# Kernel tuning notes

Hardware: AMD Instinct MI355X
Metric: run time of the kernel (lower is better)

Reference implementation:

```python
import jax, jax.numpy as jnp
import numpy as np

SEQ = 4096
EMB = 1024
OUT = 1024


def setup_inputs() -> dict:
    key = jax.random.key(0)
    k_x, k_q, k_k, k_v = jax.random.split(key, 4)
    scale = 1.0 / np.sqrt(EMB)
    inputs = jax.random.normal(k_x, (SEQ, EMB), dtype=jnp.float32)
    # torch Linear weight is (out_features, in_features); y = x @ W.T
    W_Q = jax.random.normal(k_q, (OUT, EMB), dtype=jnp.float32) * scale
    W_K = jax.random.normal(k_k, (OUT, EMB), dtype=jnp.float32) * scale
    W_V = jax.random.normal(k_v, (OUT, EMB), dtype=jnp.float32) * scale
    return {"inputs": inputs, "W_Q": W_Q, "W_K": W_K, "W_V": W_V}


def reference(inputs, W_Q, W_K, W_V):
    # projections: (S, E) @ (E, D) -> (S, D)
    q = inputs @ W_Q.T
    k = inputs @ W_K.T
    v = inputs @ W_V.T
    d_k = k.shape[-1]
    scores = (q @ k.T) / jnp.sqrt(jnp.asarray(d_k, dtype=q.dtype))  # (S, S)
    weights = jax.nn.softmax(scores, axis=-1)
    return weights @ v  # (S, D)
```

## Files before the change

kernel.cpp:

```cpp
#include <hip/hip_runtime.h>

typedef __bf16 bf16;
typedef __bf16 bf16x4 __attribute__((ext_vector_type(4)));
typedef __bf16 bf16x8 __attribute__((ext_vector_type(8)));
typedef float f32x4 __attribute__((ext_vector_type(4)));

#define SEQ 4096
#define EMB 1024

#define MODE_BF16 0
#define MODE_EXP  1
#define MODE_PART 2

__device__ __forceinline__ void async_copy16(void* lds, const void* g) {
    __builtin_amdgcn_global_load_lds(
        (const __attribute__((address_space(1))) unsigned int*)g,
        (__attribute__((address_space(3))) unsigned int*)lds,
        16, 0, 0);
}

__global__ __launch_bounds__(256) void prep_all(const float* __restrict__ x,
                                                const float* __restrict__ wq,
                                                const float* __restrict__ wk,
                                                const float* __restrict__ wv,
                                                bf16* __restrict__ xb,
                                                bf16* __restrict__ wqk,
                                                bf16* __restrict__ wvb,
                                                float* __restrict__ rowsum)
{
    const int u = blockIdx.x * 256 + threadIdx.x;
    const float* src;
    bf16* dst;
    int off;
    if (u < 1048576)      { src = x;  dst = xb;               off = u; }
    else if (u < 1310720) { src = wq; dst = wqk;              off = u - 1048576; }
    else if (u < 1572864) { src = wk; dst = wqk + EMB * EMB;  off = u - 1310720; }
    else if (u < 1835008) { src = wv; dst = wvb;              off = u - 1572864; }
    else {
        *(float4*)(rowsum + (size_t)(u - 1835008) * 4) = float4{0.f, 0.f, 0.f, 0.f};
        return;
    }
    float4 f = *(const float4*)(src + (size_t)off * 4);
    bf16x4 v = { (bf16)f.x, (bf16)f.y, (bf16)f.z, (bf16)f.w };
    *(bf16x4*)(dst + (size_t)off * 4) = v;
}

template<int OUT_MODE>
__global__ __launch_bounds__(256) void gemm_bt(const bf16* __restrict__ A,
                                               const bf16* __restrict__ B,
                                               void* __restrict__ Cv,
                                               float* __restrict__ aux,
                                               int lda, int ldb, int ldc, int K)
{
    __shared__ __align__(16) bf16 As[128 * 64];
    __shared__ __align__(16) bf16 Bs[128 * 64];

    const int tid  = threadIdx.x;
    const int lane = tid & 63;
    const int wave = tid >> 6;
    const int m0 = blockIdx.y * 128;
    const int n0 = blockIdx.x * 128;
    const size_t koff = (size_t)blockIdx.z * K;

    const int srow = tid >> 3;
    const int spc  = tid & 7;
    const int sl   = (spc - (srow & 7)) & 7;

    const int wm = (wave & 1) << 6;
    const int wn = (wave >> 1) << 6;
    const int fr = lane & 15;
    const int q  = lane >> 4;

    f32x4 acc[4][4];
    for (int i = 0; i < 4; i++)
        for (int j = 0; j < 4; j++)
            acc[i][j] = {0.f, 0.f, 0.f, 0.f};

    const bf16* Ab = A + (size_t)(m0 + srow) * lda + koff + sl * 8;
    const bf16* Bb = B + (size_t)(n0 + srow) * ldb + koff + sl * 8;

    bf16* AsD = &As[srow * 64 + spc * 8];
    bf16* BsD = &Bs[srow * 64 + spc * 8];

    const int pc0 = ((q + fr) & 7) * 8;
    const int pc1 = (((q + fr) & 7) ^ 4) * 8;

    for (int k0 = 0; k0 < K; k0 += 64) {
        __syncthreads();
        for (int t = 0; t < 4; t++) {
            async_copy16(AsD + t * 2048, Ab + k0 + (size_t)(32 * t) * lda);
            async_copy16(BsD + t * 2048, Bb + k0 + (size_t)(32 * t) * ldb);
        }
        __syncthreads();

        bf16x8 af[4], bg[4];
        for (int i = 0; i < 4; i++)
            af[i] = *(const bf16x8*)&As[(wm + i * 16 + fr) * 64 + pc0];
        for (int j = 0; j < 4; j++)
            bg[j] = *(const bf16x8*)&Bs[(wn + j * 16 + fr) * 64 + pc0];
        for (int i = 0; i < 4; i++)
            for (int j = 0; j < 4; j++)
                acc[i][j] = __builtin_amdgcn_mfma_f32_16x16x32_bf16(af[i], bg[j], acc[i][j], 0, 0, 0);
        for (int i = 0; i < 4; i++)
            af[i] = *(const bf16x8*)&As[(wm + i * 16 + fr) * 64 + pc1];
        for (int j = 0; j < 4; j++)
            bg[j] = *(const bf16x8*)&Bs[(wn + j * 16 + fr) * 64 + pc1];
        for (int i = 0; i < 4; i++)
            for (int j = 0; j < 4; j++)
                acc[i][j] = __builtin_amdgcn_mfma_f32_16x16x32_bf16(af[i], bg[j], acc[i][j], 0, 0, 0);
    }

    const int cm = m0 + wm + (q << 2);
    const int cn = n0 + wn + fr;
    if (OUT_MODE == MODE_BF16) {
        bf16* C = (bf16*)Cv;
        for (int i = 0; i < 4; i++)
            for (int j = 0; j < 4; j++)
                for (int r = 0; r < 4; r++)
                    C[(size_t)(cm + i * 16 + r) * ldc + (cn + j * 16)] = (bf16)acc[i][j][r];
    } else if (OUT_MODE == MODE_EXP) {
        bf16* C = (bf16*)Cv;
        float rs[4][4];
        for (int i = 0; i < 4; i++)
            for (int r = 0; r < 4; r++) rs[i][r] = 0.f;
        for (int i = 0; i < 4; i++)
            for (int j = 0; j < 4; j++)
                for (int r = 0; r < 4; r++) {
                    float e = __expf(acc[i][j][r] * 0.03125f);
                    C[(size_t)(cm + i * 16 + r) * ldc + (cn + j * 16)] = (bf16)e;
                    rs[i][r] += e;
                }
        for (int i = 0; i < 4; i++)
            for (int r = 0; r < 4; r++)
                for (int m = 1; m < 16; m <<= 1)
                    rs[i][r] += __shfl_xor(rs[i][r], m);
        if (fr == 0)
            for (int i = 0; i < 4; i++)
                for (int r = 0; r < 4; r++)
                    unsafeAtomicAdd(&aux[cm + i * 16 + r], rs[i][r]);
    } else {
        float* C = (blockIdx.z == 0) ? (float*)Cv
                                     : aux + (size_t)(blockIdx.z - 1) * SEQ * 1024;
        for (int i = 0; i < 4; i++)
            for (int j = 0; j < 4; j++)
                for (int r = 0; r < 4; r++)
                    C[(size_t)(cm + i * 16 + r) * ldc + (cn + j * 16)] = acc[i][j][r];
    }
}

__global__ __launch_bounds__(256) void reduce_norm(float* __restrict__ out,
                                                   const float* __restrict__ p1,
                                                   const float* __restrict__ p2,
                                                   const float* __restrict__ p3,
                                                   const float* __restrict__ rowsum)
{
    const int m = blockIdx.x;
    const float inv = 1.f / rowsum[m];
    const size_t off = (size_t)m * 1024 + threadIdx.x * 4;
    float4 a = *(const float4*)(out + off);
    float4 b = *(const float4*)(p1 + off);
    float4 c = *(const float4*)(p2 + off);
    float4 d = *(const float4*)(p3 + off);
    float4 o;
    o.x = (a.x + b.x + c.x + d.x) * inv;
    o.y = (a.y + b.y + c.y + d.y) * inv;
    o.z = (a.z + b.z + c.z + d.z) * inv;
    o.w = (a.w + b.w + c.w + d.w) * inv;
    *(float4*)(out + off) = o;
}

extern "C" void kernel_launch(void* const* d_in, const int* in_sizes, int n_in,
                              void* d_out, int out_size, void* d_ws, size_t ws_size,
                              hipStream_t stream)
{
    const float* x  = (const float*)d_in[0];
    const float* wq = (const float*)d_in[1];
    const float* wk = (const float*)d_in[2];
    const float* wv = (const float*)d_in[3];
    float* out = (float*)d_out;

    char* ws = (char*)d_ws;
    const size_t MB = 1024 * 1024;
    bf16*  E   = (bf16*)(ws);
    float* p1  = (float*)(ws + 32 * MB);
    float* p2  = (float*)(ws + 48 * MB);
    float* p3  = (float*)(ws + 64 * MB);
    bf16*  xb  = (bf16*)(ws + 32 * MB);
    bf16*  wqk = (bf16*)(ws + 40 * MB);
    bf16*  wvb = (bf16*)(ws + 44 * MB);
    bf16*  QK  = (bf16*)(ws + 64 * MB);
    bf16*  VT  = (bf16*)(ws + 80 * MB);
    float* rsm = (float*)(ws + 88 * MB);

    dim3 blk(256);

    prep_all<<<dim3(7172), blk, 0, stream>>>(x, wq, wk, wv, xb, wqk, wvb, rsm);

    gemm_bt<MODE_BF16><<<dim3(16, 32), blk, 0, stream>>>(xb, wqk, QK, nullptr,
                                                         1024, 1024, 2048, 1024);
    gemm_bt<MODE_BF16><<<dim3(32, 8), blk, 0, stream>>>(wvb, xb, VT, nullptr,
                                                        1024, 1024, 4096, 1024);
    gemm_bt<MODE_EXP><<<dim3(32, 32), blk, 0, stream>>>(QK, QK + 1024, E, rsm,
                                                        2048, 2048, 4096, 1024);
    gemm_bt<MODE_PART><<<dim3(8, 32, 4), blk, 0, stream>>>(E, VT, out, p1,
                                                           4096, 4096, 1024, 1024);
    reduce_norm<<<dim3(4096), blk, 0, stream>>>(out, p1, p2, p3, rsm);
}
```

Baseline: 248.2 us.

## Merge projection GEMMs and move softmax row sums into PV GEMM

Combines the QK and V projection GEMMs into one launch by dispatching on blockIdx.y. The exp GEMM no longer computes row sums with shuffles and atomics. Instead, the PV GEMM accumulates row sums of E from the A fragments it already loads, but only in y==0 blocks and the first two waves. The grid of the exp and PV kernels is also reordered so that M varies fastest. This cuts one launch and the epilogue reduction work in the large exp kernel, at the cost of some extra VALU adds in a subset of PV blocks.

Measured after the change: 215.9 us. -13.0%, faster.

```diff
diff --git a/kernel.cpp b/kernel.cpp
--- a/kernel.cpp
+++ b/kernel.cpp
@@ -7,10 +7,6 @@
 
 #define SEQ 4096
 #define EMB 1024
-
-#define MODE_BF16 0
-#define MODE_EXP  1
-#define MODE_PART 2
 
 __device__ __forceinline__ void async_copy16(void* lds, const void* g) {
     __builtin_amdgcn_global_load_lds(
@@ -45,45 +41,39 @@
     *(bf16x4*)(dst + (size_t)off * 4) = v;
 }
 
-template<int OUT_MODE>
-__global__ __launch_bounds__(256) void gemm_bt(const bf16* __restrict__ A,
-                                               const bf16* __restrict__ B,
-                                               void* __restrict__ Cv,
-                                               float* __restrict__ aux,
-                                               int lda, int ldb, int ldc, int K)
-{
-    __shared__ __align__(16) bf16 As[128 * 64];
-    __shared__ __align__(16) bf16 Bs[128 * 64];
-
+template<bool RSUM>
+__device__ __forceinline__ void gemm_core(const bf16* __restrict__ A,
+                                          const bf16* __restrict__ B,
+                                          int lda, int ldb, int K, long koff,
+                                          int m0, int n0,
+                                          bf16* __restrict__ As, bf16* __restrict__ Bs,
+                                          f32x4 (&acc)[4][4], float (&rsum)[4],
+                                          bool rs_active)
+{
     const int tid  = threadIdx.x;
     const int lane = tid & 63;
     const int wave = tid >> 6;
-    const int m0 = blockIdx.y * 128;
-    const int n0 = blockIdx.x * 128;
-    const size_t koff = (size_t)blockIdx.z * K;
-
     const int srow = tid >> 3;
     const int spc  = tid & 7;
     const int sl   = (spc - (srow & 7)) & 7;
-
     const int wm = (wave & 1) << 6;
     const int wn = (wave >> 1) << 6;
     const int fr = lane & 15;
     const int q  = lane >> 4;
 
-    f32x4 acc[4][4];
     for (int i = 0; i < 4; i++)
         for (int j = 0; j < 4; j++)
             acc[i][j] = {0.f, 0.f, 0.f, 0.f};
+    if (RSUM)
+        for (int i = 0; i < 4; i++) rsum[i] = 0.f;
 
     const bf16* Ab = A + (size_t)(m0 + srow) * lda + koff + sl * 8;
     const bf16* Bb = B + (size_t)(n0 + srow) * ldb + koff + sl * 8;
-
     bf16* AsD = &As[srow * 64 + spc * 8];
     bf16* BsD = &Bs[srow * 64 + spc * 8];
 
     const int pc0 = ((q + fr) & 7) * 8;
-    const int pc1 = (((q + fr) & 7) ^ 4) * 8;
+    const int pc1 = pc0 ^ 32;
 
     for (int k0 = 0; k0 < K; k0 += 64) {
         __syncthreads();
@@ -98,54 +88,123 @@
             af[i] = *(const bf16x8*)&As[(wm + i * 16 + fr) * 64 + pc0];
         for (int j = 0; j < 4; j++)
             bg[j] = *(const bf16x8*)&Bs[(wn + j * 16 + fr) * 64 + pc0];
+        if (RSUM && rs_active)
+            for (int i = 0; i < 4; i++)
+                for (int e = 0; e < 8; e++) rsum[i] += (float)af[i][e];
         for (int i = 0; i < 4; i++)
             for (int j = 0; j < 4; j++)
                 acc[i][j] = __builtin_amdgcn_mfma_f32_16x16x32_bf16(af[i], bg[j], acc[i][j], 0, 0, 0);
+
         for (int i = 0; i < 4; i++)
             af[i] = *(const bf16x8*)&As[(wm + i * 16 + fr) * 64 + pc1];
         for (int j = 0; j < 4; j++)
             bg[j] = *(const bf16x8*)&Bs[(wn + j * 16 + fr) * 64 + pc1];
+        if (RSUM && rs_active)
+            for (int i = 0; i < 4; i++)
+                for (int e = 0; e < 8; e++) rsum[i] += (float)af[i][e];
         for (int i = 0; i < 4; i++)
             for (int j = 0; j < 4; j++)
                 acc[i][j] = __builtin_amdgcn_mfma_f32_16x16x32_bf16(af[i], bg[j], acc[i][j], 0, 0, 0);
     }
-
-    const int cm = m0 + wm + (q << 2);
-    const int cn = n0 + wn + fr;
-    if (OUT_MODE == MODE_BF16) {
-        bf16* C = (bf16*)Cv;
-        for (int i = 0; i < 4; i++)
-            for (int j = 0; j < 4; j++)
-                for (int r = 0; r < 4; r++)
-                    C[(size_t)(cm + i * 16 + r) * ldc + (cn + j * 16)] = (bf16)acc[i][j][r];
-    } else if (OUT_MODE == MODE_EXP) {
-        bf16* C = (bf16*)Cv;
-        float rs[4][4];
-        for (int i = 0; i < 4; i++)
-            for (int r = 0; r < 4; r++) rs[i][r] = 0.f;
-        for (int i = 0; i < 4; i++)
-            for (int j = 0; j < 4; j++)
-                for (int r = 0; r < 4; r++) {
-                    float e = __expf(acc[i][j][r] * 0.03125f);
-                    C[(size_t)(cm + i * 16 + r) * ldc + (cn + j * 16)] = (bf16)e;
-                    rs[i][r] += e;
-                }
-        for (int i = 0; i < 4; i++)
+}
+
+__global__ __launch_bounds__(256) void gemm_proj(const bf16* __restrict__ xb,
+                                                 const bf16* __restrict__ wqk,
+                                                 const bf16* __restrict__ wvb,
+                                                 bf16* __restrict__ QK,
+                                                 bf16* __restrict__ VT)
+{
+    __shared__ __align__(16) bf16 As[128 * 64];
+    __shared__ __align__(16) bf16 Bs[128 * 64];
+
+    const bf16 *A, *B;
+    bf16* C;
+    int ldc, m0, n0;
+    if (blockIdx.y < 16) {
+        A = xb; B = wqk; C = QK; ldc = 2048;
+        m0 = blockIdx.x * 128; n0 = blockIdx.y * 128;
+    } else {
+        A = wvb; B = xb; C = VT; ldc = 4096;
+        m0 = (blockIdx.x & 7) * 128;
+        n0 = ((blockIdx.x >> 3) + ((blockIdx.y - 16) << 2)) * 128;
+    }
+
+    f32x4 acc[4][4];
+    float rs[4];
+    gemm_core<false>(A, B, 1024, 1024, 1024, 0, m0, n0, As, Bs, acc, rs, false);
+
+    const int lane = threadIdx.x & 63;
+    const int wave = threadIdx.x >> 6;
+    const int cm = m0 + ((wave & 1) << 6) + ((lane >> 4) << 2);
+    const int cn = n0 + ((wave >> 1) << 6) + (lane & 15);
+    for (int i = 0; i < 4; i++)
+        for (int j = 0; j < 4; j++)
             for (int r = 0; r < 4; r++)
-                for (int m = 1; m < 16; m <<= 1)
-                    rs[i][r] += __shfl_xor(rs[i][r], m);
-        if (fr == 0)
+                C[(size_t)(cm + i * 16 + r) * ldc + (cn + j * 16)] = (bf16)acc[i][j][r];
+}
+
+__global__ __launch_bounds__(256) void gemm_exp(const bf16* __restrict__ QK,
+                                                bf16* __restrict__ E)
+{
+    __shared__ __align__(16) bf16 As[128 * 64];
+    __shared__ __align__(16) bf16 Bs[128 * 64];
+
+    const int m0 = blockIdx.x * 128;
+    const int n0 = blockIdx.y * 128;
+    f32x4 acc[4][4];
+    float rs[4];
+    gemm_core<false>(QK, QK + 1024, 2048, 2048, 1024, 0, m0, n0, As, Bs, acc, rs, false);
+
+    const int lane = threadIdx.x & 63;
+    const int wave = threadIdx.x >> 6;
+    const int cm = m0 + ((wave & 1) << 6) + ((lane >> 4) << 2);
+    const int cn = n0 + ((wave >> 1) << 6) + (lane & 15);
+    for (int i = 0; i < 4; i++)
+        for (int j = 0; j < 4; j++)
+            for (int r = 0; r < 4; r++)
+                E[(size_t)(cm + i * 16 + r) * 4096 + (cn + j * 16)] =
+                    (bf16)__expf(acc[i][j][r] * 0.03125f);
+}
+
+__global__ __launch_bounds__(256) void gemm_pv(const bf16* __restrict__ E,
+                                               const bf16* __restrict__ VT,
+                                               float* __restrict__ out,
+                                               float* __restrict__ p1,
+                                               float* __restrict__ rowsum)
+{
+    __shared__ __align__(16) bf16 As[128 * 64];
+    __shared__ __align__(16) bf16 Bs[128 * 64];
+
+    const int m0 = blockIdx.x * 128;
+    const int n0 = blockIdx.y * 128;
+    const long koff = (long)blockIdx.z * 1024;
+    const bool rs_active = (blockIdx.y == 0) && (threadIdx.x < 128);
+
+    f32x4 acc[4][4];
+    float rs[4];
+    gemm_core<true>(E, VT, 4096, 4096, 1024, koff, m0, n0, As, Bs, acc, rs, rs_active);
+
+    const int lane = threadIdx.x & 63;
+    const int wave = threadIdx.x >> 6;
+    if (rs_active) {
+        for (int i = 0; i < 4; i++) {
+            rs[i] += __shfl_xor(rs[i], 16);
+            rs[i] += __shfl_xor(rs[i], 32);
+        }
+        if (lane < 16) {
+            const int wm = (wave & 1) << 6;
             for (int i = 0; i < 4; i++)
-                for (int r = 0; r < 4; r++)
-                    unsafeAtomicAdd(&aux[cm + i * 16 + r], rs[i][r]);
-    } else {
-        float* C = (blockIdx.z == 0) ? (float*)Cv
-                                     : aux + (size_t)(blockIdx.z - 1) * SEQ * 1024;
-        for (int i = 0; i < 4; i++)
-            for (int j = 0; j < 4; j++)
-                for (int r = 0; r < 4; r++)
-                    C[(size_t)(cm + i * 16 + r) * ldc + (cn + j * 16)] = acc[i][j][r];
-    }
+                unsafeAtomicAdd(&rowsum[m0 + wm + i * 16 + lane], rs[i]);
+        }
+    }
+
+    float* C = (blockIdx.z == 0) ? out : p1 + (size_t)(blockIdx.z - 1) * SEQ * 1024;
+    const int cm = m0 + ((wave & 1) << 6) + ((lane >> 4) << 2);
+    const int cn = n0 + ((wave >> 1) << 6) + (lane & 15);
+    for (int i = 0; i < 4; i++)
+        for (int j = 0; j < 4; j++)
+            for (int r = 0; r < 4; r++)
+                C[(size_t)(cm + i * 16 + r) * 1024 + (cn + j * 16)] = acc[i][j][r];
 }
 
 __global__ __launch_bounds__(256) void reduce_norm(float* __restrict__ out,
@@ -195,14 +254,8 @@
     dim3 blk(256);
 
     prep_all<<<dim3(7172), blk, 0, stream>>>(x, wq, wk, wv, xb, wqk, wvb, rsm);
-
-    gemm_bt<MODE_BF16><<<dim3(16, 32), blk, 0, stream>>>(xb, wqk, QK, nullptr,
-                                                         1024, 1024, 2048, 1024);
-    gemm_bt<MODE_BF16><<<dim3(32, 8), blk, 0, stream>>>(wvb, xb, VT, nullptr,
-                                                        1024, 1024, 4096, 1024);
-    gemm_bt<MODE_EXP><<<dim3(32, 32), blk, 0, stream>>>(QK, QK + 1024, E, rsm,
-                                                        2048, 2048, 4096, 1024);
-    gemm_bt<MODE_PART><<<dim3(8, 32, 4), blk, 0, stream>>>(E, VT, out, p1,
-                                                           4096, 4096, 1024, 1024);
+    gemm_proj<<<dim3(32, 24), blk, 0, stream>>>(xb, wqk, wvb, QK, VT);
+    gemm_exp<<<dim3(32, 32), blk, 0, stream>>>(QK, E);
+    gemm_pv<<<dim3(32, 8, 4), blk, 0, stream>>>(E, VT, out, p1, rsm);
     reduce_norm<<<dim3(4096), blk, 0, stream>>>(out, p1, p2, p3, rsm);
 }
```
